# Optimization experiments

Hardware: AMD Instinct MI355X
Metric: run time of the kernel (lower is better)

Reference implementation:

```python
import jax, jax.numpy as jnp
import numpy as np

N = 100000        # num nodes
E = 1600000       # num edges (before self-loops)
F_IN = 128        # num_node_features
HEADS = 8
HID = 8           # per-head hidden channels in conv1 (hardcoded in module)
C = 16            # num_classes
NEG_SLOPE = 0.2   # PyG GATConv default


def setup_inputs() -> dict:
    key = jax.random.key(0)
    ks = jax.random.split(key, 10)
    x = jax.random.normal(ks[0], (N, F_IN), jnp.float32)
    edge_index = jax.random.randint(ks[1], (2, E), 0, N, dtype=jnp.int32)
    s1 = 1.0 / np.sqrt(F_IN)
    s2 = 1.0 / np.sqrt(HEADS * HID)
    W1 = jax.random.normal(ks[2], (F_IN, HEADS * HID), jnp.float32) * s1
    att_src1 = jax.random.normal(ks[3], (HEADS, HID), jnp.float32) * s1
    att_dst1 = jax.random.normal(ks[4], (HEADS, HID), jnp.float32) * s1
    b1 = jnp.zeros((HEADS * HID,), jnp.float32)
    W2 = jax.random.normal(ks[5], (HEADS * HID, C), jnp.float32) * s2
    att_src2 = jax.random.normal(ks[6], (1, C), jnp.float32) * s2
    att_dst2 = jax.random.normal(ks[7], (1, C), jnp.float32) * s2
    b2 = jnp.zeros((C,), jnp.float32)
    return {"x": x, "edge_index": edge_index, "W1": W1, "att_src1": att_src1,
            "att_dst1": att_dst1, "b1": b1, "W2": W2, "att_src2": att_src2,
            "att_dst2": att_dst2, "b2": b2}


def gat_conv(x, edge_index, W, att_src, att_dst, bias, heads, out_ch, concat):
    """PyG-style GATConv (eval mode; add_self_loops=True)."""
    n = x.shape[0]
    loop = jnp.arange(n, dtype=edge_index.dtype)
    src = jnp.concatenate([edge_index[0], loop])   # message source j
    dst = jnp.concatenate([edge_index[1], loop])   # message target i
    h = (x @ W).reshape(n, heads, out_ch)          # [N, H, O]
    a_s = jnp.einsum('nho,ho->nh', h, att_src)     # [N, H]
    a_d = jnp.einsum('nho,ho->nh', h, att_dst)
    e = jax.nn.leaky_relu(a_s[src] + a_d[dst], NEG_SLOPE)     # [E', H]
    m = jax.lax.stop_gradient(jax.ops.segment_max(e, dst, num_segments=n))
    ex = jnp.exp(e - m[dst])
    denom = jax.ops.segment_sum(ex, dst, num_segments=n)      # [N, H]
    alpha = ex / (denom[dst] + 1e-16)                         # [E', H]
    out = jax.ops.segment_sum(h[src] * alpha[:, :, None], dst, num_segments=n)
    out = out.reshape(n, heads * out_ch) if concat else out.mean(axis=1)
    return out + bias


def reference(x, edge_index, W1, att_src1, att_dst1, b1, W2, att_src2, att_dst2, b2):
    h = gat_conv(x, edge_index, W1, att_src1, att_dst1, b1, HEADS, HID, True)
    h = jax.nn.relu(h)  # dropout is identity in eval mode
    out = gat_conv(h, edge_index, W2, att_src2, att_dst2, b2, 1, C, False)
    return jax.nn.log_softmax(out, axis=1)
```

## Files before the change

### kernel.cpp

```cpp
#include <hip/hip_runtime.h>
#include <hip/hip_bf16.h>

#define NN 100000
#define FIN 128
#define H8 64
#define NC 16
#define BKS 9
#define BMASK 511
#define CHUNK 8192

typedef unsigned short ushort_t;
typedef unsigned int uint_t;

__device__ __forceinline__ float bu2f(ushort_t u) {
    unsigned v = ((unsigned)u) << 16;
    return __uint_as_float(v);
}
__device__ __forceinline__ ushort_t f2bu(float f) {
    __hip_bfloat16 h = __float2bfloat16(f);
    return *reinterpret_cast<ushort_t*>(&h);
}
__device__ __forceinline__ float dot4(float4 a, float4 b) {
    return a.x * b.x + a.y * b.y + a.z * b.z + a.w * b.w;
}
__device__ __forceinline__ void fma4(float4& a, float s, float4 w) {
    a.x += s * w.x; a.y += s * w.y; a.z += s * w.z; a.w += s * w.w;
}


__device__ __forceinline__ void gemm1_body(int gb,
        const float* __restrict__ x, const float* __restrict__ W,
        const float* __restrict__ attS, const float* __restrict__ attD,
        ushort_t* __restrict__ h1b, float* __restrict__ as1,
        float* __restrict__ ad1, int n, float* ws) {
    int t = threadIdx.x;
    const float4* W4 = (const float4*)W;
    float4* ws4 = (float4*)ws;
    for (int j = t; j < FIN * H8 / 4; j += 256) ws4[j] = W4[j];
    __syncthreads();

    int wv = t >> 6, lane = t & 63;
    int ng = lane >> 4, cg = lane & 15;
    int node0 = (gb * 4 + wv) * 16 + ng * 4;

    int r0 = min(node0 + 0, n - 1), r1 = min(node0 + 1, n - 1);
    int r2 = min(node0 + 2, n - 1), r3 = min(node0 + 3, n - 1);
    const float* xp0 = x + (long)r0 * FIN;
    const float* xp1 = x + (long)r1 * FIN;
    const float* xp2 = x + (long)r2 * FIN;
    const float* xp3 = x + (long)r3 * FIN;

    float4 a0 = {0, 0, 0, 0}, a1 = {0, 0, 0, 0}, a2 = {0, 0, 0, 0}, a3 = {0, 0, 0, 0};
#pragma unroll 2
    for (int k = 0; k < FIN; k += 4) {
        float4 xa = *(const float4*)(xp0 + k);
        float4 xb = *(const float4*)(xp1 + k);
        float4 xc = *(const float4*)(xp2 + k);
        float4 xd = *(const float4*)(xp3 + k);
        float4 w0 = *(const float4*)(ws + (k + 0) * H8 + cg * 4);
        float4 w1 = *(const float4*)(ws + (k + 1) * H8 + cg * 4);
        float4 w2 = *(const float4*)(ws + (k + 2) * H8 + cg * 4);
        float4 w3 = *(const float4*)(ws + (k + 3) * H8 + cg * 4);
        fma4(a0, xa.x, w0); fma4(a0, xa.y, w1); fma4(a0, xa.z, w2); fma4(a0, xa.w, w3);
        fma4(a1, xb.x, w0); fma4(a1, xb.y, w1); fma4(a1, xb.z, w2); fma4(a1, xb.w, w3);
        fma4(a2, xc.x, w0); fma4(a2, xc.y, w1); fma4(a2, xc.z, w2); fma4(a2, xc.w, w3);
        fma4(a3, xd.x, w0); fma4(a3, xd.y, w1); fma4(a3, xd.z, w2); fma4(a3, xd.w, w3);
    }

    float4 sA = *(const float4*)(attS + cg * 4);
    float4 dA = *(const float4*)(attD + cg * 4);
    float4 av[4] = {a0, a1, a2, a3};
#pragma unroll
    for (int j = 0; j < 4; ++j) {
        int node = node0 + j;
        float4 a = av[j];
        float vs = dot4(a, sA);
        float vd = dot4(a, dA);
        vs += __shfl_xor(vs, 1, 64);
        vd += __shfl_xor(vd, 1, 64);
        if (node < n) {
            ushort4 q;
            q.x = f2bu(a.x); q.y = f2bu(a.y); q.z = f2bu(a.z); q.w = f2bu(a.w);
            *(ushort4*)(h1b + (long)node * H8 + cg * 4) = q;
            if ((lane & 1) == 0) {
                as1[node * 8 + (cg >> 1)] = vs;
                ad1[node * 8 + (cg >> 1)] = vd;
            }
        }
    }
}

__device__ __forceinline__ void binA_body(int cb, const int* __restrict__ dst,
        int* __restrict__ bh, int e, int nb, int nblk, int* hist) {
    int t = threadIdx.x;
    hist[t] = 0;
    __syncthreads();
    int base = cb * CHUNK;
    int endj = min(base + CHUNK, e);
    for (int k0 = base + t * 4; k0 < endj; k0 += 1024) {
        if (k0 + 3 < endj) {
            int4 d4 = *(const int4*)(dst + k0);
            atomicAdd(&hist[d4.x >> BKS], 1);
            atomicAdd(&hist[d4.y >> BKS], 1);
            atomicAdd(&hist[d4.z >> BKS], 1);
            atomicAdd(&hist[d4.w >> BKS], 1);
        } else {
            for (int k = k0; k < endj; ++k) atomicAdd(&hist[dst[k] >> BKS], 1);
        }
    }
    __syncthreads();
    if (t < nb) bh[t * nblk + cb] = hist[t];
}

__device__ __forceinline__ void scanB_body(int j, int* __restrict__ bh,
        int* __restrict__ btot, int nblk, int* ts) {
    int t = threadIdx.x;
    int v = (t < nblk) ? bh[j * nblk + t] : 0;
    ts[t] = v;
    __syncthreads();
    int run = v;
    for (int off = 1; off < 256; off <<= 1) {
        int y = (t >= off) ? ts[t - off] : 0;
        __syncthreads();
        run += y;
        ts[t] = run;
        __syncthreads();
    }
    if (t < nblk) bh[j * nblk + t] = run - v;
    if (t == 255) btot[j] = run;
}

__device__ __forceinline__ void binC_body(int cb, const int* __restrict__ src,
        const int* __restrict__ dst, const int* __restrict__ bh,
        const int* __restrict__ bstart, uint_t* __restrict__ binned,
        int e, int nb, int nblk, int* off) {
    int t = threadIdx.x;
    if (t < nb) off[t] = bh[t * nblk + cb] + bstart[t];
    __syncthreads();
    int base = cb * CHUNK;
    int endj = min(base + CHUNK, e);
    for (int k0 = base + t * 4; k0 < endj; k0 += 1024) {
        if (k0 + 3 < endj) {
            int4 d4 = *(const int4*)(dst + k0);
            int4 s4 = *(const int4*)(src + k0);
            int p0 = atomicAdd(&off[d4.x >> BKS], 1);
            binned[p0] = ((uint_t)(d4.x & BMASK) << 17) | (uint_t)s4.x;
            int p1 = atomicAdd(&off[d4.y >> BKS], 1);
            binned[p1] = ((uint_t)(d4.y & BMASK) << 17) | (uint_t)s4.y;
            int p2 = atomicAdd(&off[d4.z >> BKS], 1);
            binned[p2] = ((uint_t)(d4.z & BMASK) << 17) | (uint_t)s4.z;
            int p3 = atomicAdd(&off[d4.w >> BKS], 1);
            binned[p3] = ((uint_t)(d4.w & BMASK) << 17) | (uint_t)s4.w;
        } else {
            for (int k = k0; k < endj; ++k) {
                int d = dst[k], s = src[k];
                int p = atomicAdd(&off[d >> BKS], 1);
                binned[p] = ((uint_t)(d & BMASK) << 17) | (uint_t)s;
            }
        }
    }
}


__global__ __launch_bounds__(256) void k_fuseA(const int* __restrict__ dst,
        int* __restrict__ bh, int e, int nb, int nblk,
        const float* __restrict__ x, const float* __restrict__ W,
        const float* __restrict__ attS, const float* __restrict__ attD,
        ushort_t* __restrict__ h1b, float* __restrict__ as1,
        float* __restrict__ ad1, int n) {
    __shared__ float smem[FIN * H8];
    if ((int)blockIdx.x < nblk)
        binA_body(blockIdx.x, dst, bh, e, nb, nblk, (int*)smem);
    else
        gemm1_body(blockIdx.x - nblk, x, W, attS, attD, h1b, as1, ad1, n, smem);
}

__global__ __launch_bounds__(256) void k_fuseB(int* __restrict__ bh,
        int* __restrict__ btot, int nblk, int nb, int g1ofs,
        const float* __restrict__ x, const float* __restrict__ W,
        const float* __restrict__ attS, const float* __restrict__ attD,
        ushort_t* __restrict__ h1b, float* __restrict__ as1,
        float* __restrict__ ad1, int n) {
    __shared__ float smem[FIN * H8];
    if ((int)blockIdx.x < nb)
        scanB_body(blockIdx.x, bh, btot, nblk, (int*)smem);
    else
        gemm1_body(g1ofs + blockIdx.x - nb, x, W, attS, attD, h1b, as1, ad1, n, smem);
}

__global__ __launch_bounds__(256) void k_fuseC(const int* __restrict__ src,
        const int* __restrict__ dst, const int* __restrict__ bh,
        const int* __restrict__ bstart, uint_t* __restrict__ binned,
        int e, int nb, int nblk, int g1ofs,
        const float* __restrict__ x, const float* __restrict__ W,
        const float* __restrict__ attS, const float* __restrict__ attD,
        ushort_t* __restrict__ h1b, float* __restrict__ as1,
        float* __restrict__ ad1, int n) {
    __shared__ float smem[FIN * H8];
    if ((int)blockIdx.x < nblk)
        binC_body(blockIdx.x, src, dst, bh, bstart, binned, e, nb, nblk, (int*)smem);
    else
        gemm1_body(g1ofs + blockIdx.x - nblk, x, W, attS, attD, h1b, as1, ad1, n, smem);
}

__global__ __launch_bounds__(256) void k_scanT(const int* __restrict__ btot,
        int* __restrict__ bstart, int nb) {
    __shared__ int ts[256];
    int j = threadIdx.x;
    int s = (j < nb) ? btot[j] : 0;
    ts[j] = s;
    __syncthreads();
    int run = s;
    for (int off = 1; off < 256; off <<= 1) {
        int y = (j >= off) ? ts[j - off] : 0;
        __syncthreads();
        run += y;
        ts[j] = run;
        __syncthreads();
    }
    if (j < nb) bstart[j] = run - s;
    if (j == nb - 1) bstart[nb] = run;
}

__global__ __launch_bounds__(256) void k_bucket(const uint_t* __restrict__ binned,
        const int* __restrict__ bstart, int* __restrict__ rp, int* __restrict__ col,
        int e, int n, int nb) {
    __shared__ int deg[512];
    __shared__ int ts[256];
    int b = blockIdx.x, t = threadIdx.x;
    int node0 = b << BKS;
    int S = bstart[b];
    int Se = bstart[b + 1];
    deg[t] = 0; deg[t + 256] = 0;
    __syncthreads();
    for (int k = S + t; k < Se; k += 256)
        atomicAdd(&deg[binned[k] >> 17], 1);
    __syncthreads();
    int g0 = node0 + 2 * t, g1 = g0 + 1;
    int c0 = (g0 < n) ? deg[2 * t] + 1 : 0;
    int c1 = (g1 < n) ? deg[2 * t + 1] + 1 : 0;
    int s = c0 + c1;
    ts[t] = s;
    __syncthreads();
    int run = s;
    for (int off = 1; off < 256; off <<= 1) {
        int y = (t >= off) ? ts[t - off] : 0;
        __syncthreads();
        run += y;
        ts[t] = run;
        __syncthreads();
    }
    int ex = run - s;
    int base = S + node0;
    int p0 = base + ex, p1 = base + ex + c0;
    if (g0 < n) { rp[g0] = p0; col[p0] = g0; deg[2 * t] = p0 + 1; }
    if (g1 < n) { rp[g1] = p1; col[p1] = g1; deg[2 * t + 1] = p1 + 1; }
    if (b == nb - 1 && t == 0) rp[n] = e + n;
    __syncthreads();
    for (int k = S + t; k < Se; k += 256) {
        uint_t pk = binned[k];
        int dLow = pk >> 17;
        int sv = (int)(pk & 0x1FFFFu);
        int p = atomicAdd(&deg[dLow], 1);
        col[p] = sv;
    }
}


__global__ __launch_bounds__(256) void k_agg1(const int* __restrict__ rp,
        const int* __restrict__ col, const ushort_t* __restrict__ h1b,
        const float* __restrict__ as1, const float* __restrict__ ad1,
        const float* __restrict__ b1, ushort_t* __restrict__ z1b, int n) {
    int w = (blockIdx.x * 256 + threadIdx.x) >> 6;
    int lane = threadIdx.x & 63;
    int iA = w * 2, iB = iA + 1;
    if (iA >= n) return;
    bool hasB = (iB < n);
    int slot = lane >> 3;
    int h2 = lane & 7;
    int l16 = lane & 15;
    int begA = rp[iA], endA = rp[iA + 1];
    int begB = hasB ? rp[iB] : 0, endB = hasB ? rp[iB + 1] : 0;
    int lastA = endA - 1, lastB = endB - 1;
    float adiA = ad1[iA * 8 + h2];
    float adiB = hasB ? ad1[iB * 8 + h2] : 0.f;
    float denA = 0.f, denB = 0.f;
    float numA[8] = {0.f, 0.f, 0.f, 0.f, 0.f, 0.f, 0.f, 0.f};
    float numB[8] = {0.f, 0.f, 0.f, 0.f, 0.f, 0.f, 0.f, 0.f};
    int roundsA = (endA - begA + 15) >> 4;
    int roundsB = hasB ? ((endB - begB + 15) >> 4) : 0;
    int rmax = max(roundsA, roundsB);
    int vA = col[min(begA + l16, lastA)];
    int vB = roundsB ? col[min(begB + l16, lastB)] : 0;
    for (int r = 0; r < rmax; ++r) {
        bool mA = r < roundsA, mB = r < roundsB;
        int kA0 = begA + r * 16, kB0 = begB + r * 16;
        int vnA = 0, vnB = 0;
        if (r + 1 < roundsA) vnA = col[min(kA0 + 16 + l16, lastA)];
        if (r + 1 < roundsB) vnB = col[min(kB0 + 16 + l16, lastB)];
        float pAa = 0.f, pAb = 0.f, pBa = 0.f, pBb = 0.f;
        uint4 uaA, ubA, uaB, ubB;
        if (mA) {
            int s0 = __shfl(vA, slot, 64);
            int s1 = __shfl(vA, 8 + slot, 64);
            float sv0 = as1[s0 * 8 + h2];
            float sv1 = as1[s1 * 8 + h2];
            uaA = *((const uint4*)(h1b + ((size_t)(unsigned)s0 << 6)) + h2);
            ubA = *((const uint4*)(h1b + ((size_t)(unsigned)s1 << 6)) + h2);
            float e0 = sv0 + adiA;
            e0 = fmaxf(e0, 0.f) + 0.2f * fminf(e0, 0.f);
            pAa = (kA0 + slot < endA) ? __expf(e0) : 0.f;
            float e1 = sv1 + adiA;
            e1 = fmaxf(e1, 0.f) + 0.2f * fminf(e1, 0.f);
            pAb = (kA0 + 8 + slot < endA) ? __expf(e1) : 0.f;
            denA += pAa + pAb;
        }
        if (mB) {
            int s0 = __shfl(vB, slot, 64);
            int s1 = __shfl(vB, 8 + slot, 64);
            float sv0 = as1[s0 * 8 + h2];
            float sv1 = as1[s1 * 8 + h2];
            uaB = *((const uint4*)(h1b + ((size_t)(unsigned)s0 << 6)) + h2);
            ubB = *((const uint4*)(h1b + ((size_t)(unsigned)s1 << 6)) + h2);
            float e0 = sv0 + adiB;
            e0 = fmaxf(e0, 0.f) + 0.2f * fminf(e0, 0.f);
            pBa = (kB0 + slot < endB) ? __expf(e0) : 0.f;
            float e1 = sv1 + adiB;
            e1 = fmaxf(e1, 0.f) + 0.2f * fminf(e1, 0.f);
            pBb = (kB0 + 8 + slot < endB) ? __expf(e1) : 0.f;
            denB += pBa + pBb;
        }
#define ACC8(NUM, P, U)                                                    \
        {                                                                  \
            NUM[0] += (P) * __uint_as_float((U).x << 16);                  \
            NUM[1] += (P) * __uint_as_float((U).x & 0xffff0000u);          \
            NUM[2] += (P) * __uint_as_float((U).y << 16);                  \
            NUM[3] += (P) * __uint_as_float((U).y & 0xffff0000u);          \
            NUM[4] += (P) * __uint_as_float((U).z << 16);                  \
            NUM[5] += (P) * __uint_as_float((U).z & 0xffff0000u);          \
            NUM[6] += (P) * __uint_as_float((U).w << 16);                  \
            NUM[7] += (P) * __uint_as_float((U).w & 0xffff0000u);          \
        }
        if (mA) { ACC8(numA, pAa, uaA) ACC8(numA, pAb, ubA) }
        if (mB) { ACC8(numB, pBa, uaB) ACC8(numB, pBb, ubB) }
#undef ACC8
        vA = vnA; vB = vnB;
    }
#pragma unroll
    for (int q = 0; q < 8; ++q) {
        numA[q] += __shfl_xor(numA[q], 8, 64);
        numA[q] += __shfl_xor(numA[q], 16, 64);
        numA[q] += __shfl_xor(numA[q], 32, 64);
        numB[q] += __shfl_xor(numB[q], 8, 64);
        numB[q] += __shfl_xor(numB[q], 16, 64);
        numB[q] += __shfl_xor(numB[q], 32, 64);
    }
    denA += __shfl_xor(denA, 8, 64);
    denA += __shfl_xor(denA, 16, 64);
    denA += __shfl_xor(denA, 32, 64);
    denB += __shfl_xor(denB, 8, 64);
    denB += __shfl_xor(denB, 16, 64);
    denB += __shfl_xor(denB, 32, 64);
    if (lane < 16) {
        bool isB = lane >= 8;
        if (!isB || hasB) {
            int node = isB ? iB : iA;
            const float* nm = isB ? numB : numA;
            float invd = 1.0f / ((isB ? denB : denA) + 1e-16f);
            float4 b0 = *(const float4*)(b1 + h2 * 8);
            float4 b1v = *(const float4*)(b1 + h2 * 8 + 4);
            float o0 = fmaxf(nm[0] * invd + b0.x, 0.f);
            float o1 = fmaxf(nm[1] * invd + b0.y, 0.f);
            float o2 = fmaxf(nm[2] * invd + b0.z, 0.f);
            float o3 = fmaxf(nm[3] * invd + b0.w, 0.f);
            float o4 = fmaxf(nm[4] * invd + b1v.x, 0.f);
            float o5 = fmaxf(nm[5] * invd + b1v.y, 0.f);
            float o6 = fmaxf(nm[6] * invd + b1v.z, 0.f);
            float o7 = fmaxf(nm[7] * invd + b1v.w, 0.f);
            uint4 q;
            q.x = (uint_t)f2bu(o0) | ((uint_t)f2bu(o1) << 16);
            q.y = (uint_t)f2bu(o2) | ((uint_t)f2bu(o3) << 16);
            q.z = (uint_t)f2bu(o4) | ((uint_t)f2bu(o5) << 16);
            q.w = (uint_t)f2bu(o6) | ((uint_t)f2bu(o7) << 16);
            *(uint4*)(z1b + (size_t)node * H8 + h2 * 8) = q;
        }
    }
}


__global__ __launch_bounds__(256) void k_gemm2(const ushort_t* __restrict__ z1b,
        const float* __restrict__ W2, const float* __restrict__ attS,
        const float* __restrict__ attD, ushort_t* __restrict__ h2b,
        float* __restrict__ as2, float* __restrict__ ad2) {
    __shared__ float ws[H8 * NC];
    __shared__ float zs[16][H8 + 1];
    int t = threadIdx.x;
    for (int j = t; j < H8 * NC; j += 256) ws[j] = W2[j];
    int n0 = blockIdx.x * 16;
    {
        const ushort4* zp = (const ushort4*)(z1b + (size_t)n0 * H8);
        ushort4 q = zp[t];
        int r = t >> 4, k2 = (t & 15) * 4;
        zs[r][k2 + 0] = bu2f(q.x);
        zs[r][k2 + 1] = bu2f(q.y);
        zs[r][k2 + 2] = bu2f(q.z);
        zs[r][k2 + 3] = bu2f(q.w);
    }
    __syncthreads();
    int c = t & 15, g = t >> 4;
    float acc = 0.f;
#pragma unroll 8
    for (int k = 0; k < H8; ++k) acc += zs[g][k] * ws[k * NC + c];
    h2b[(long)(n0 + g) * NC + c] = f2bu(acc);
    float vs = acc * attS[c], vd = acc * attD[c];
    for (int off = 1; off < 16; off <<= 1) {
        vs += __shfl_xor(vs, off, 64);
        vd += __shfl_xor(vd, off, 64);
    }
    if (c == 0) { as2[n0 + g] = vs; ad2[n0 + g] = vd; }
}


__global__ __launch_bounds__(256) void k_agg2(const int* __restrict__ rp,
        const int* __restrict__ col, const ushort_t* __restrict__ h2b,
        const float* __restrict__ as2, const float* __restrict__ ad2,
        const float* __restrict__ b2, float* __restrict__ out, int n) {
    int i = (blockIdx.x * 256 + threadIdx.x) >> 6;
    int lane = threadIdx.x & 63;
    if (i >= n) return;
    int grp = lane >> 3;
    int cp = lane & 7;
    int beg = rp[i], end = rp[i + 1];
    int last = end - 1;
    int deg = end - beg;
    float adi = ad2[i];
    const uint_t* h2u = (const uint_t*)h2b;
    float denp = 0.f, nx = 0.f, ny = 0.f;
    int rounds = (deg + 31) >> 5;
    for (int r = 0; r < rounds; ++r) {
        int k = beg + r * 32;
        int rem = end - k;
        int v = col[min(k + (lane & 31), last)];
        float sv = as2[v];
        float e = sv + adi;
        e = fmaxf(e, 0.f) + 0.2f * fminf(e, 0.f);
        int lim = min(rem, 32);
        float p = (lane < lim) ? __expf(e) : 0.f;
        denp += p;
#define AGG2_PAIR(S0, S1)                                                  \
        {                                                                  \
            int i0 = (S0) * 8 + grp, i1 = (S1) * 8 + grp;                  \
            int r0 = __shfl(v, i0, 64), r1 = __shfl(v, i1, 64);            \
            float q0 = __shfl(p, i0, 64), q1 = __shfl(p, i1, 64);          \
            uint_t u0 = h2u[((size_t)(unsigned)r0 << 3) + cp];             \
            uint_t u1 = h2u[((size_t)(unsigned)r1 << 3) + cp];             \
            nx += q0 * __uint_as_float(u0 << 16);                          \
            ny += q0 * __uint_as_float(u0 & 0xffff0000u);                  \
            nx += q1 * __uint_as_float(u1 << 16);                          \
            ny += q1 * __uint_as_float(u1 & 0xffff0000u);                  \
        }
        AGG2_PAIR(0, 1)
        if (lim > 16) AGG2_PAIR(2, 3)
#undef AGG2_PAIR
    }
    nx += __shfl_xor(nx, 8, 64);  ny += __shfl_xor(ny, 8, 64);
    nx += __shfl_xor(nx, 16, 64); ny += __shfl_xor(ny, 16, 64);
    nx += __shfl_xor(nx, 32, 64); ny += __shfl_xor(ny, 32, 64);
    denp += __shfl_xor(denp, 1, 64);
    denp += __shfl_xor(denp, 2, 64);
    denp += __shfl_xor(denp, 4, 64);
    denp += __shfl_xor(denp, 8, 64);
    denp += __shfl_xor(denp, 16, 64);
    denp += __shfl_xor(denp, 32, 64);
    float invd = 1.0f / (denp + 1e-16f);
    float2 bp = ((const float2*)b2)[cp];
    float ox = nx * invd + bp.x;
    float oy = ny * invd + bp.y;
    float mx = fmaxf(ox, oy);
    mx = fmaxf(mx, __shfl_xor(mx, 1, 64));
    mx = fmaxf(mx, __shfl_xor(mx, 2, 64));
    mx = fmaxf(mx, __shfl_xor(mx, 4, 64));
    float sm = __expf(ox - mx) + __expf(oy - mx);
    sm += __shfl_xor(sm, 1, 64);
    sm += __shfl_xor(sm, 2, 64);
    sm += __shfl_xor(sm, 4, 64);
    float lg = mx + __logf(sm);
    if (lane < 8) {
        float2 res = {ox - lg, oy - lg};
        ((float2*)(out + (size_t)i * NC))[cp] = res;
    }
}


extern "C" void kernel_launch(void* const* d_in, const int* in_sizes, int n_in,
                              void* d_out, int out_size, void* d_ws, size_t ws_size,
                              hipStream_t stream) {
    const float* x     = (const float*)d_in[0];
    const int*   ei    = (const int*)d_in[1];
    const float* W1    = (const float*)d_in[2];
    const float* attS1 = (const float*)d_in[3];
    const float* attD1 = (const float*)d_in[4];
    const float* b1    = (const float*)d_in[5];
    const float* W2    = (const float*)d_in[6];
    const float* attS2 = (const float*)d_in[7];
    const float* attD2 = (const float*)d_in[8];
    const float* b2    = (const float*)d_in[9];
    float* out = (float*)d_out;

    const int N = NN;
    const int E = in_sizes[1] / 2;
    const int NB = (N + (1 << BKS) - 1) >> BKS;
    const int NBLK = (E + CHUNK - 1) / CHUNK;

    ushort_t* z1b = (ushort_t*)d_ws;
    float* as1 = (float*)(z1b + (size_t)N * H8);
    float* ad1 = as1 + (size_t)N * 8;
    float* as2 = ad1 + (size_t)N * 8;
    float* ad2 = as2 + N;
    ushort_t* h1b = (ushort_t*)(ad2 + N);
    ushort_t* h2b = h1b + (size_t)N * H8;
    int* rp   = (int*)(h2b + (size_t)N * NC);
    int* col  = rp + (N + 1);
    int* bh   = col + (E + N);
    int* btot = bh + (size_t)NB * NBLK;
    int* bstart = btot + NB;
    uint_t* binned = (uint_t*)z1b;

    const int* srcp = ei;
    const int* dstp = ei + E;

    const int G1 = (N + 63) / 64;
    const int G1A = G1 * 1 / 3;
    const int G1B = G1 * 1 / 3;
    const int G1C = G1 - G1A - G1B;

    k_fuseA<<<NBLK + G1A, 256, 0, stream>>>(dstp, bh, E, NB, NBLK,
            x, W1, attS1, attD1, h1b, as1, ad1, N);
    k_fuseB<<<NB + G1B, 256, 0, stream>>>(bh, btot, NBLK, NB, G1A,
            x, W1, attS1, attD1, h1b, as1, ad1, N);
    k_scanT<<<1, 256, 0, stream>>>(btot, bstart, NB);
    k_fuseC<<<NBLK + G1C, 256, 0, stream>>>(srcp, dstp, bh, bstart, binned,
            E, NB, NBLK, G1A + G1B, x, W1, attS1, attD1, h1b, as1, ad1, N);
    k_bucket<<<NB, 256, 0, stream>>>(binned, bstart, rp, col, E, N, NB);

    k_agg1<<<(N + 7) / 8, 256, 0, stream>>>(rp, col, h1b, as1, ad1, b1, z1b, N);
    k_gemm2<<<N / 16, 256, 0, stream>>>(z1b, W2, attS2, attD2, h2b, as2, ad2);
    k_agg2<<<(N + 3) / 4, 256, 0, stream>>>(rp, col, h2b, as2, ad2, b2, out, N);
}
```

Baseline: 179.5 us.

## Fuse layer-2 projection and attention logits into layer-1 aggregation kernel

Removes the separate k_gemm2 kernel. After aggregating layer 1, each wave now applies bias and ReLU, multiplies by W2 (staged in padded shared memory), reduces with cross-lane shuffles, and writes h2b, as2 and ad2 directly. This avoids writing and re-reading the z1 intermediate in bf16 and saves one kernel launch. In exchange each agg1 block loads W2 into shared memory, issues extra shuffles and uses more registers. Because the projection now uses the fp32 activations, rounding differs slightly from before.

```diff
diff --git a/kernel.cpp b/kernel.cpp
--- a/kernel.cpp
+++ b/kernel.cpp
@@ -270,7 +270,22 @@
 __global__ __launch_bounds__(256) void k_agg1(const int* __restrict__ rp,
         const int* __restrict__ col, const ushort_t* __restrict__ h1b,
         const float* __restrict__ as1, const float* __restrict__ ad1,
-        const float* __restrict__ b1, ushort_t* __restrict__ z1b, int n) {
+        const float* __restrict__ b1, const float* __restrict__ W2,
+        const float* __restrict__ attS2, const float* __restrict__ attD2,
+        ushort_t* __restrict__ h2b, float* __restrict__ as2,
+        float* __restrict__ ad2, int n) {
+    __shared__ float w2s[H8 * 17];
+    __shared__ float s2s[NC], d2s[NC];
+    {
+        int t = threadIdx.x;
+        for (int j = t; j < H8 * NC; j += 256) {
+            int ch = j >> 4, c = j & 15;
+            w2s[ch * 17 + c] = W2[j];
+        }
+        if (t < NC) { s2s[t] = attS2[t]; d2s[t] = attD2[t]; }
+    }
+    __syncthreads();
+
     int w = (blockIdx.x * 256 + threadIdx.x) >> 6;
     int lane = threadIdx.x & 63;
     int iA = w * 2, iB = iA + 1;
@@ -361,63 +376,58 @@
     denB += __shfl_xor(denB, 8, 64);
     denB += __shfl_xor(denB, 16, 64);
     denB += __shfl_xor(denB, 32, 64);
-    if (lane < 16) {
-        bool isB = lane >= 8;
-        if (!isB || hasB) {
-            int node = isB ? iB : iA;
-            const float* nm = isB ? numB : numA;
-            float invd = 1.0f / ((isB ? denB : denA) + 1e-16f);
-            float4 b0 = *(const float4*)(b1 + h2 * 8);
-            float4 b1v = *(const float4*)(b1 + h2 * 8 + 4);
-            float o0 = fmaxf(nm[0] * invd + b0.x, 0.f);
-            float o1 = fmaxf(nm[1] * invd + b0.y, 0.f);
-            float o2 = fmaxf(nm[2] * invd + b0.z, 0.f);
-            float o3 = fmaxf(nm[3] * invd + b0.w, 0.f);
-            float o4 = fmaxf(nm[4] * invd + b1v.x, 0.f);
-            float o5 = fmaxf(nm[5] * invd + b1v.y, 0.f);
-            float o6 = fmaxf(nm[6] * invd + b1v.z, 0.f);
-            float o7 = fmaxf(nm[7] * invd + b1v.w, 0.f);
-            uint4 q;
-            q.x = (uint_t)f2bu(o0) | ((uint_t)f2bu(o1) << 16);
-            q.y = (uint_t)f2bu(o2) | ((uint_t)f2bu(o3) << 16);
-            q.z = (uint_t)f2bu(o4) | ((uint_t)f2bu(o5) << 16);
-            q.w = (uint_t)f2bu(o6) | ((uint_t)f2bu(o7) << 16);
-            *(uint4*)(z1b + (size_t)node * H8 + h2 * 8) = q;
-        }
-    }
-}
-
-
-__global__ __launch_bounds__(256) void k_gemm2(const ushort_t* __restrict__ z1b,
-        const float* __restrict__ W2, const float* __restrict__ attS,
-        const float* __restrict__ attD, ushort_t* __restrict__ h2b,
-        float* __restrict__ as2, float* __restrict__ ad2) {
-    __shared__ float ws[H8 * NC];
-    __shared__ float zs[16][H8 + 1];
-    int t = threadIdx.x;
-    for (int j = t; j < H8 * NC; j += 256) ws[j] = W2[j];
-    int n0 = blockIdx.x * 16;
-    {
-        const ushort4* zp = (const ushort4*)(z1b + (size_t)n0 * H8);
-        ushort4 q = zp[t];
-        int r = t >> 4, k2 = (t & 15) * 4;
-        zs[r][k2 + 0] = bu2f(q.x);
-        zs[r][k2 + 1] = bu2f(q.y);
-        zs[r][k2 + 2] = bu2f(q.z);
-        zs[r][k2 + 3] = bu2f(q.w);
-    }
-    __syncthreads();
-    int c = t & 15, g = t >> 4;
-    float acc = 0.f;
-#pragma unroll 8
-    for (int k = 0; k < H8; ++k) acc += zs[g][k] * ws[k * NC + c];
-    h2b[(long)(n0 + g) * NC + c] = f2bu(acc);
-    float vs = acc * attS[c], vd = acc * attD[c];
-    for (int off = 1; off < 16; off <<= 1) {
-        vs += __shfl_xor(vs, off, 64);
-        vd += __shfl_xor(vd, off, 64);
-    }
-    if (c == 0) { as2[n0 + g] = vs; ad2[n0 + g] = vd; }
+    float invdA = 1.0f / (denA + 1e-16f);
+    float invdB = 1.0f / (denB + 1e-16f);
+    float4 bb0 = *(const float4*)(b1 + h2 * 8);
+    float4 bb1 = *(const float4*)(b1 + h2 * 8 + 4);
+    float zA[8], zB[8];
+    zA[0] = fmaxf(numA[0] * invdA + bb0.x, 0.f);
+    zA[1] = fmaxf(numA[1] * invdA + bb0.y, 0.f);
+    zA[2] = fmaxf(numA[2] * invdA + bb0.z, 0.f);
+    zA[3] = fmaxf(numA[3] * invdA + bb0.w, 0.f);
+    zA[4] = fmaxf(numA[4] * invdA + bb1.x, 0.f);
+    zA[5] = fmaxf(numA[5] * invdA + bb1.y, 0.f);
+    zA[6] = fmaxf(numA[6] * invdA + bb1.z, 0.f);
+    zA[7] = fmaxf(numA[7] * invdA + bb1.w, 0.f);
+    zB[0] = fmaxf(numB[0] * invdB + bb0.x, 0.f);
+    zB[1] = fmaxf(numB[1] * invdB + bb0.y, 0.f);
+    zB[2] = fmaxf(numB[2] * invdB + bb0.z, 0.f);
+    zB[3] = fmaxf(numB[3] * invdB + bb0.w, 0.f);
+    zB[4] = fmaxf(numB[4] * invdB + bb1.x, 0.f);
+    zB[5] = fmaxf(numB[5] * invdB + bb1.y, 0.f);
+    zB[6] = fmaxf(numB[6] * invdB + bb1.z, 0.f);
+    zB[7] = fmaxf(numB[7] * invdB + bb1.w, 0.f);
+    int c0 = slot * 2, c1 = c0 + 1;
+    float pA0 = 0.f, pA1 = 0.f, pB0 = 0.f, pB1 = 0.f;
+#pragma unroll
+    for (int j = 0; j < 8; ++j) {
+        int ch = h2 * 8 + j;
+        float w0 = w2s[ch * 17 + c0];
+        float w1 = w2s[ch * 17 + c1];
+        pA0 += zA[j] * w0; pA1 += zA[j] * w1;
+        pB0 += zB[j] * w0; pB1 += zB[j] * w1;
+    }
+    pA0 += __shfl_xor(pA0, 1, 64); pA0 += __shfl_xor(pA0, 2, 64); pA0 += __shfl_xor(pA0, 4, 64);
+    pA1 += __shfl_xor(pA1, 1, 64); pA1 += __shfl_xor(pA1, 2, 64); pA1 += __shfl_xor(pA1, 4, 64);
+    pB0 += __shfl_xor(pB0, 1, 64); pB0 += __shfl_xor(pB0, 2, 64); pB0 += __shfl_xor(pB0, 4, 64);
+    pB1 += __shfl_xor(pB1, 1, 64); pB1 += __shfl_xor(pB1, 2, 64); pB1 += __shfl_xor(pB1, 4, 64);
+    float vsA = pA0 * s2s[c0] + pA1 * s2s[c1];
+    float vdA = pA0 * d2s[c0] + pA1 * d2s[c1];
+    float vsB = pB0 * s2s[c0] + pB1 * s2s[c1];
+    float vdB = pB0 * d2s[c0] + pB1 * d2s[c1];
+    vsA += __shfl_xor(vsA, 8, 64); vsA += __shfl_xor(vsA, 16, 64); vsA += __shfl_xor(vsA, 32, 64);
+    vdA += __shfl_xor(vdA, 8, 64); vdA += __shfl_xor(vdA, 16, 64); vdA += __shfl_xor(vdA, 32, 64);
+    vsB += __shfl_xor(vsB, 8, 64); vsB += __shfl_xor(vsB, 16, 64); vsB += __shfl_xor(vsB, 32, 64);
+    vdB += __shfl_xor(vdB, 8, 64); vdB += __shfl_xor(vdB, 16, 64); vdB += __shfl_xor(vdB, 32, 64);
+    if (h2 == 0) {
+        uint_t qw = (uint_t)f2bu(pA0) | ((uint_t)f2bu(pA1) << 16);
+        ((uint_t*)(h2b + (size_t)iA * NC))[slot] = qw;
+    } else if (h2 == 1 && hasB) {
+        uint_t qw = (uint_t)f2bu(pB0) | ((uint_t)f2bu(pB1) << 16);
+        ((uint_t*)(h2b + (size_t)iB * NC))[slot] = qw;
+    }
+    if (lane == 0) { as2[iA] = vsA; ad2[iA] = vdA; }
+    if (lane == 1 && hasB) { as2[iB] = vsB; ad2[iB] = vdB; }
 }
 
 
@@ -543,7 +553,7 @@
             E, NB, NBLK, G1A + G1B, x, W1, attS1, attD1, h1b, as1, ad1, N);
     k_bucket<<<NB, 256, 0, stream>>>(binned, bstart, rp, col, E, N, NB);
 
-    k_agg1<<<(N + 7) / 8, 256, 0, stream>>>(rp, col, h1b, as1, ad1, b1, z1b, N);
-    k_gemm2<<<N / 16, 256, 0, stream>>>(z1b, W2, attS2, attD2, h2b, as2, ad2);
+    k_agg1<<<(N + 7) / 8, 256, 0, stream>>>(rp, col, h1b, as1, ad1, b1,
+            W2, attS2, attD2, h2b, as2, ad2, N);
     k_agg2<<<(N + 3) / 4, 256, 0, stream>>>(rp, col, h2b, as2, ad2, b2, out, N);
 }
```

Result: slower. 185.6 us (+3.4%).
